# Performance work log

Hardware: AMD Instinct MI355X
Metric: run time of the kernel (lower is better)

## Reference

```python
import jax, jax.numpy as jnp
import numpy as np
from jax import lax


def _conv_layer(x, K, k, stride, pad):
    """Faithful reimplementation of the custom Conv2d, including its two quirks:
    1) weight/input flatten-order mismatch: K.reshape(k*k*cin, cout) pairs flat
       index m (decoded as kh,kw,cin for K) against x flattened as (cin,kh,kw),
       so the effective conv weight is K.reshape(-1,cout).reshape(cin,k,k,cout).
    2) the python loop range(0, padd-k, stride) misses the last valid position
       whenever (padd-k) is divisible by stride, leaving last row/col zero.
    """
    B, cin, s_in, _ = x.shape
    cout = K.shape[-1]
    out_size = (s_in + 2 * pad - k) // stride + 1
    padd = s_in + 2 * pad
    n_loop = -(-(padd - k) // stride)  # = len(range(0, padd-k, stride))
    xp = jnp.pad(x, ((0, 0), (0, 0), (pad, pad), (pad, pad))) if pad > 0 else x
    # effective weight honoring the flatten-order mismatch: (cin, kh, kw, cout)
    W = K.reshape(-1, cout).reshape(cin, k, k, cout)
    y = lax.conv_general_dilated(
        xp, W, window_strides=(stride, stride), padding='VALID',
        dimension_numbers=('NCHW', 'IHWO', 'NCHW'))
    n = min(n_loop, out_size)
    out = jnp.zeros((B, cout, out_size, out_size), x.dtype)
    out = out.at[:, :, :n, :n].set(y[:, :, :n, :n])
    return out


def setup_inputs() -> dict:
    key = jax.random.key(0)
    ks = jax.random.split(key, 9)
    NUM_CLASSES = 10
    B = 8192

    def kinit(k_, shape):
        fan_in = shape[1] * int(np.prod(shape[2:]))  # torch fan_in for 4D
        bound = float(np.sqrt(6.0 / fan_in))
        return jax.random.uniform(k_, shape, jnp.float32, -bound, bound)

    x = jax.random.normal(ks[0], (B, 3, 28, 28), jnp.float32)
    K1 = kinit(ks[1], (5, 5, 3, 8))
    K2 = kinit(ks[2], (3, 3, 8, 16))
    K3 = kinit(ks[3], (3, 3, 16, 16))
    K4 = kinit(ks[4], (3, 3, 16, 16))
    K5 = kinit(ks[5], (3, 3, 16, 16))
    K6 = kinit(ks[6], (5, 5, 16, 32))
    fc_in = 6 * 6 * 32  # 1152
    bw = float(np.sqrt(1.0 / fc_in))
    Wfc = jax.random.uniform(ks[7], (NUM_CLASSES, fc_in), jnp.float32, -bw, bw)
    bfc = jax.random.uniform(ks[8], (NUM_CLASSES,), jnp.float32, -bw, bw)
    return {"x": x, "K1": K1, "K2": K2, "K3": K3, "K4": K4, "K5": K5,
            "K6": K6, "Wfc": Wfc, "bfc": bfc}


def reference(x, K1, K2, K3, K4, K5, K6, Wfc, bfc):
    h = jax.nn.relu(_conv_layer(x, K1, 5, 2, 1))   # (B,8,13,13)
    h = jax.nn.relu(_conv_layer(h, K2, 3, 1, 1))   # (B,16,13,13), last row/col zero
    h = jax.nn.relu(_conv_layer(h, K3, 3, 1, 1))
    h = jax.nn.relu(_conv_layer(h, K4, 3, 1, 1))
    h = jax.nn.relu(_conv_layer(h, K5, 3, 1, 1))
    h = _conv_layer(h, K6, 5, 2, 1)                # (B,32,6,6), last row/col zero
    flat = h.reshape(h.shape[0], -1)               # (B,1152)
    logits = flat @ Wfc.T + bfc
    return jax.nn.softmax(logits, axis=1)
```

## Files before the change

kernel.cpp:

```cpp
#include <hip/hip_runtime.h>
#include <math.h>

#define TPB 256

typedef __attribute__((ext_vector_type(8))) short short8;
typedef __attribute__((ext_vector_type(4))) float f32x4;
typedef unsigned short u16;

__device__ __forceinline__ f32x4 MFMA(short8 a, short8 b, f32x4 c) {
    return __builtin_amdgcn_mfma_f32_16x16x32_bf16(a, b, c, 0, 0, 0);
}
__device__ __forceinline__ u16 f2bf(float f) {
    unsigned int u = __builtin_bit_cast(unsigned int, f);
    u += 0x7FFFu + ((u >> 16) & 1u);
    return (u16)(u >> 16);
}
__device__ __forceinline__ float bf2f(u16 h) {
    unsigned int u = ((unsigned int)h) << 16;
    return __builtin_bit_cast(float, u);
}

extern "C" __global__ void prep_w(const float* __restrict__ K2, const float* __restrict__ K3,
                                  const float* __restrict__ K4, const float* __restrict__ K5,
                                  const float* __restrict__ K6, short8* __restrict__ W)
{
    const int slot = blockIdx.x * blockDim.x + threadIdx.x;
    if (slot >= 5632) return;
    const int lane = slot & 63;
    const int ent  = slot >> 6;
    const int o    = lane & 15;
    const int lhi  = lane >> 4;
    float w[8];
    int hl;
    if (ent < 6) {
        const int s = ent >> 1; hl = ent & 1;
        const int t = s * 4 + lhi;
#pragma unroll
        for (int j = 0; j < 8; j++)
            w[j] = (t < 9) ? K2[(j * 9 + t) * 16 + o] : 0.f;
    } else if (ent < 36) {
        const int e  = ent - 6;
        const float* Kg = (e < 10) ? K3 : (e < 20) ? K4 : K5;
        const int el = e % 10;
        const int s  = el >> 1; hl = el & 1;
        const int chalf = (lhi & 1) * 8;
        const int t = 2 * s + (lhi >> 1);
#pragma unroll
        for (int j = 0; j < 8; j++)
            w[j] = (t < 9) ? Kg[((chalf + j) * 9 + t) * 16 + o] : 0.f;
    } else {
        const int e = ent - 36;
        const int s = e >> 2; hl = (e >> 1) & 1;
        const int nh = e & 1;
        const int chalf = (lhi & 1) * 8;
        const int t  = 2 * s + (lhi >> 1);
        const int oo = nh * 16 + o;
#pragma unroll
        for (int j = 0; j < 8; j++)
            w[j] = (t < 25) ? K6[((chalf + j) * 25 + t) * 32 + oo] : 0.f;
    }
    short8 v;
#pragma unroll
    for (int j = 0; j < 8; j++) {
        const u16 h = f2bf(w[j]);
        v[j] = hl ? (short)f2bf(w[j] - bf2f(h)) : (short)h;
    }
    W[slot] = v;
}


__device__ __forceinline__ void conv8(const u16* __restrict__ s0,
                                      u16* __restrict__ d0,
                                      const short8* __restrict__ Wt,
                                      int wave, int lane, int rot)
{
    const int o   = lane & 15;
    const int lhi = lane >> 4;
    short8 Bhi[3], Blo[3];
#pragma unroll
    for (int s = 0; s < 3; s++) {
        Bhi[s] = Wt[(s * 2 + 0) * 64 + lane];
        Blo[s] = Wt[(s * 2 + 1) * 64 + lane];
    }
    const u16* sl = s0 + 3600;
    const int r0 = lane & 15;

    auto tile = [&](int m) {
        const int p  = m * 16 + r0;
        const int ip = (p * 683) >> 13;
        const int jp = p - 12 * ip;
        f32x4 acc = {0.f, 0.f, 0.f, 0.f};
#pragma unroll
        for (int s = 0; s < 3; s++) {
            const int t  = s * 4 + lhi;
            const int tt = t > 8 ? 8 : t;
            const int kh = (tt * 11) >> 5;
            const int kw = tt - 3 * kh;
            const int px = (ip + kh) * 15 + (jp + kw);
            const short8 Ahi = *(const short8*)(s0 + px * 8);
            const short8 Alo = *(const short8*)(sl + px * 8);
            acc = MFMA(Ahi, Bhi[s], acc);
            acc = MFMA(Alo, Bhi[s], acc);
            acc = MFMA(Ahi, Blo[s], acc);
        }
        const int p0 = m * 16 + lhi * 4;
#pragma unroll
        for (int r = 0; r < 4; r++) {
            const int pp = p0 + r;
            const int ii = (pp * 683) >> 13;
            const int jj = pp - 12 * ii;
            const float v = fmaxf(acc[r], 0.f);
            const u16 h = f2bf(v);
            const int px2 = (ii + 1) * 15 + (jj + 1);
            const int da  = (o >> 3) * 1800 + px2 * 8 + (o & 7);
            d0[da]        = h;
            d0[da + 3600] = f2bf(v - bf2f(h));
        }
    };
    const int m0 = (wave + rot) & 3;
    tile(m0);
    tile(m0 + 4);
    if (m0 == 0) tile(8);
}

__device__ __forceinline__ void conv16(const u16* __restrict__ s0,
                                       u16* __restrict__ d0,
                                       const short8* __restrict__ Wt,
                                       int wave, int lane, int rot)
{
    const int o    = lane & 15;
    const int lhi  = lane >> 4;
    const int hsel = lhi & 1;
    const int tsel = lhi >> 1;
    short8 Bhi[5], Blo[5];
#pragma unroll
    for (int s = 0; s < 5; s++) {
        Bhi[s] = Wt[(s * 2 + 0) * 64 + lane];
        Blo[s] = Wt[(s * 2 + 1) * 64 + lane];
    }
    const u16* sh = s0 + hsel * 1800;
    const u16* sl = sh + 3600;
    const int r0 = lane & 15;

    auto tile = [&](int m) {
        const int p  = m * 16 + r0;
        const int ip = (p * 683) >> 13;
        const int jp = p - 12 * ip;
        f32x4 acc = {0.f, 0.f, 0.f, 0.f};
#pragma unroll
        for (int s = 0; s < 5; s++) {
            const int t  = 2 * s + tsel;
            const int tt = t > 8 ? 8 : t;
            const int kh = (tt * 11) >> 5;
            const int kw = tt - 3 * kh;
            const int px = (ip + kh) * 15 + (jp + kw);
            const short8 Ahi = *(const short8*)(sh + px * 8);
            const short8 Alo = *(const short8*)(sl + px * 8);
            acc = MFMA(Ahi, Bhi[s], acc);
            acc = MFMA(Alo, Bhi[s], acc);
            acc = MFMA(Ahi, Blo[s], acc);
        }
        const int p0 = m * 16 + lhi * 4;
#pragma unroll
        for (int r = 0; r < 4; r++) {
            const int pp = p0 + r;
            const int ii = (pp * 683) >> 13;
            const int jj = pp - 12 * ii;
            const float v = fmaxf(acc[r], 0.f);
            const u16 h = f2bf(v);
            const int px2 = (ii + 1) * 15 + (jj + 1);
            const int da  = (o >> 3) * 1800 + px2 * 8 + (o & 7);
            d0[da]        = h;
            d0[da + 3600] = f2bf(v - bf2f(h));
        }
    };
    const int m0 = (wave + rot) & 3;
    tile(m0);
    tile(m0 + 4);
    if (m0 == 0) tile(8);
}

extern "C" __global__ void __launch_bounds__(TPB)
cnn_fused(const float* __restrict__ xg, const float* __restrict__ K1,
          const float* __restrict__ Wfc, const float* __restrict__ bfc,
          const short8* __restrict__ W, float* __restrict__ out)
{
    __shared__ __align__(16) unsigned char smem[28864];
    u16*   const Ah   = (u16*)smem;
    u16*   const Bh   = (u16*)(smem + 14400);
    float* const sX   = (float*)(smem + 14400);
    float* const sF   = (float*)(smem + 14400);
    float* const sLog = (float*)(smem + 28800);
    uint4* const z4   = (uint4*)smem;
    const uint4 Z = {0u, 0u, 0u, 0u};

    const int tid  = threadIdx.x;
    const int lane = tid & 63;
    const int wave = tid >> 6;
    const int img  = blockIdx.x;

    for (int i = tid; i < 1804; i += TPB) z4[i] = Z;
    __syncthreads();

    const float4* xi4 = (const float4*)(xg + (size_t)img * 2352);
    for (int i4 = tid; i4 < 588; i4 += TPB) {
        const float4 v = xi4[i4];
        const int c = i4 / 196;
        const int rem = i4 - c * 196;
        const int r = rem / 7;
        const int q = rem - r * 7;
        float* dp = sX + c * 900 + (r + 1) * 30 + q * 4 + 1;
        dp[0] = v.x; dp[1] = v.y; dp[2] = v.z; dp[3] = v.w;
    }
    __syncthreads();

    if (tid < 208) {
        const int o  = tid & 7;
        const int jj = tid >> 3;
        const int j  = jj % 13;
        const int i0 = (jj / 13) * 7;
        float acc[7];
#pragma unroll
        for (int q = 0; q < 7; q++) acc[q] = 0.f;
#pragma unroll
        for (int c = 0; c < 3; c++) {
            const float* bp = sX + c * 900 + 2 * j;
#pragma unroll
            for (int kwp = 0; kwp < 2; kwp++) {
                float2 xr[17];
#pragma unroll
                for (int r = 0; r < 17; r++) {
                    int row = 2 * i0 + r;
                    row = row > 29 ? 29 : row;
                    xr[r] = *(const float2*)(bp + row * 30 + 2 * kwp);
                }
#pragma unroll
                for (int kh = 0; kh < 5; kh++) {
                    const float w0 = K1[(c * 25 + kh * 5 + 2 * kwp) * 8 + o];
                    const float w1 = K1[(c * 25 + kh * 5 + 2 * kwp + 1) * 8 + o];
#pragma unroll
                    for (int q = 0; q < 7; q++) {
                        acc[q] = fmaf(xr[2 * q + kh].x, w0, acc[q]);
                        acc[q] = fmaf(xr[2 * q + kh].y, w1, acc[q]);
                    }
                }
            }
            {
                float xs[17];
#pragma unroll
                for (int r = 0; r < 17; r++) {
                    int row = 2 * i0 + r;
                    row = row > 29 ? 29 : row;
                    xs[r] = bp[row * 30 + 4];
                }
#pragma unroll
                for (int kh = 0; kh < 5; kh++) {
                    const float w4 = K1[(c * 25 + kh * 5 + 4) * 8 + o];
#pragma unroll
                    for (int q = 0; q < 7; q++)
                        acc[q] = fmaf(xs[2 * q + kh], w4, acc[q]);
                }
            }
        }
#pragma unroll
        for (int q = 0; q < 7; q++) {
            const int i = i0 + q;
            if (i < 13) {
                const float v = fmaxf(acc[q], 0.f);
                const u16 h = f2bf(v);
                const int da = ((i + 1) * 15 + (j + 1)) * 8 + o;
                Ah[da]        = h;
                Ah[da + 3600] = f2bf(v - bf2f(h));
            }
        }
    }
    __syncthreads();

    for (int i = tid + 900; i < 1800; i += TPB) z4[i] = Z;
    __syncthreads();

    conv8(Ah, Bh, W, wave, lane, 0);
    __syncthreads();

    for (int i = tid; i < 900; i += TPB) z4[i] = Z;
    __syncthreads();

    conv16(Bh, Ah, W + 384, wave, lane, 1);
    __syncthreads();
    conv16(Ah, Bh, W + 1024, wave, lane, 2);
    __syncthreads();
    conv16(Bh, Ah, W + 1664, wave, lane, 3);
    __syncthreads();

    for (int i = tid + 900; i < 1188; i += TPB) z4[i] = Z;
    __syncthreads();

    {
        const short8* Wt6 = W + 2304;
        const int mt   = wave >> 1;
        const int nh   = wave & 1;
        const int lhi  = lane >> 4;
        const int hsel = lhi & 1;
        const int tsel = lhi >> 1;
        const int o    = nh * 16 + (lane & 15);
        const int pr = mt * 16 + (lane & 15);
        const int pe = pr < 25 ? pr : 0;
        const int ia = (pe * 52) >> 8;
        const int ja = pe - 5 * ia;
        const u16* sh = Ah + hsel * 1800;
        const u16* sl = sh + 3600;
        f32x4 acc = {0.f, 0.f, 0.f, 0.f};
#pragma unroll 4
        for (int s = 0; s < 13; s++) {
            const int t  = 2 * s + tsel;
            const int tt = t > 24 ? 24 : t;
            const int kh = (tt * 52) >> 8;
            const int kw = tt - 5 * kh;
            const int px = (2 * ia + kh) * 15 + (2 * ja + kw);
            const short8 Ahi = *(const short8*)(sh + px * 8);
            const short8 Alo = *(const short8*)(sl + px * 8);
            const short8 Bh2 = Wt6[((s * 2 + 0) * 2 + nh) * 64 + lane];
            const short8 Bl2 = Wt6[((s * 2 + 1) * 2 + nh) * 64 + lane];
            acc = MFMA(Ahi, Bh2, acc);
            acc = MFMA(Alo, Bh2, acc);
            acc = MFMA(Ahi, Bl2, acc);
        }
        const int p0 = mt * 16 + lhi * 4;
#pragma unroll
        for (int r = 0; r < 4; r++) {
            const int pp = p0 + r;
            if (pp < 25) {
                const int ii = (pp * 52) >> 8;
                const int jj = pp - 5 * ii;
                sF[o * 36 + ii * 6 + jj] = acc[r];
            }
        }
    }
    __syncthreads();

    if (tid < 160) {
        const int c = tid >> 4;
        const int l = tid & 15;
        const float4* fv = (const float4*)(sF + l * 72);
        const float4* wv = (const float4*)(Wfc + c * 1152 + l * 72);
        float p = 0.f;
#pragma unroll
        for (int m = 0; m < 18; m++) {
            const float4 a = fv[m];
            const float4 b = wv[m];
            p = fmaf(a.x, b.x, p);
            p = fmaf(a.y, b.y, p);
            p = fmaf(a.z, b.z, p);
            p = fmaf(a.w, b.w, p);
        }
        p += __shfl_down(p, 8, 16);
        p += __shfl_down(p, 4, 16);
        p += __shfl_down(p, 2, 16);
        p += __shfl_down(p, 1, 16);
        if (l == 0) sLog[c] = p + bfc[c];
    }
    __syncthreads();

    if (tid < 10) {
        float mx = sLog[0];
#pragma unroll
        for (int k = 1; k < 10; k++) mx = fmaxf(mx, sLog[k]);
        float s = 0.f;
#pragma unroll
        for (int k = 0; k < 10; k++) s += expf(sLog[k] - mx);
        out[(size_t)img * 10 + tid] = expf(sLog[tid] - mx) / s;
    }
}

extern "C" void kernel_launch(void* const* d_in, const int* in_sizes, int n_in,
                              void* d_out, int out_size, void* d_ws, size_t ws_size,
                              hipStream_t stream) {
    const float* x   = (const float*)d_in[0];
    const float* K1  = (const float*)d_in[1];
    const float* K2  = (const float*)d_in[2];
    const float* K3  = (const float*)d_in[3];
    const float* K4  = (const float*)d_in[4];
    const float* K5  = (const float*)d_in[5];
    const float* K6  = (const float*)d_in[6];
    const float* Wfc = (const float*)d_in[7];
    const float* bfc = (const float*)d_in[8];
    float* out = (float*)d_out;
    short8* W = (short8*)d_ws;

    prep_w<<<22, TPB, 0, stream>>>(K2, K3, K4, K5, K6, W);

    const int B = in_sizes[0] / 2352;
    cnn_fused<<<B, TPB, 0, stream>>>(x, K1, Wfc, bfc, W, out);
}
```

Measured before the change: 220.1 us.

## Move first conv layer onto bf16 split-precision MFMA with preprocessed K1 weights

Replaces the scalar FP32 FMA implementation of conv1 (5x5 stride 2, 3->8 channels) with MFMA tiles using a hi/lo bf16 split of both inputs and K1 weights. The K1 weights are packed by prep_w, and the input is stored in LDS as bf16 hi/lo planes. The LDS layout is reorganised into three buffers and some zeroing passes and barriers are removed. Shared memory grows from about 28.9KB to 40.4KB, which may reduce occupancy. Half of each MFMA's output columns and part of the K dimension are padding, so some work is wasted.

```diff
diff --git a/kernel.cpp b/kernel.cpp
--- a/kernel.cpp
+++ b/kernel.cpp
@@ -20,12 +20,13 @@
     return __builtin_bit_cast(float, u);
 }
 
-extern "C" __global__ void prep_w(const float* __restrict__ K2, const float* __restrict__ K3,
-                                  const float* __restrict__ K4, const float* __restrict__ K5,
-                                  const float* __restrict__ K6, short8* __restrict__ W)
+extern "C" __global__ void prep_w(const float* __restrict__ K1, const float* __restrict__ K2,
+                                  const float* __restrict__ K3, const float* __restrict__ K4,
+                                  const float* __restrict__ K5, const float* __restrict__ K6,
+                                  short8* __restrict__ W)
 {
     const int slot = blockIdx.x * blockDim.x + threadIdx.x;
-    if (slot >= 5632) return;
+    if (slot >= 6144) return;
     const int lane = slot & 63;
     const int ent  = slot >> 6;
     const int o    = lane & 15;
@@ -48,7 +49,7 @@
 #pragma unroll
         for (int j = 0; j < 8; j++)
             w[j] = (t < 9) ? Kg[((chalf + j) * 9 + t) * 16 + o] : 0.f;
-    } else {
+    } else if (ent < 88) {
         const int e = ent - 36;
         const int s = e >> 2; hl = (e >> 1) & 1;
         const int nh = e & 1;
@@ -58,6 +59,16 @@
 #pragma unroll
         for (int j = 0; j < 8; j++)
             w[j] = (t < 25) ? K6[((chalf + j) * 25 + t) * 32 + oo] : 0.f;
+    } else {
+        const int e = ent - 88;
+        const int s = e >> 1; hl = e & 1;
+        const int g  = s * 4 + lhi;
+        const int gc = g > 14 ? 14 : g;
+        const int c  = (gc * 52) >> 8;
+        const int kh = gc - 5 * c;
+#pragma unroll
+        for (int j = 0; j < 8; j++)
+            w[j] = (g < 15 && o < 8 && j < 5) ? K1[(c * 25 + kh * 5 + j) * 8 + o] : 0.f;
     }
     short8 v;
 #pragma unroll
@@ -181,16 +192,16 @@
 }
 
 extern "C" __global__ void __launch_bounds__(TPB)
-cnn_fused(const float* __restrict__ xg, const float* __restrict__ K1,
+cnn_fused(const float* __restrict__ xg,
           const float* __restrict__ Wfc, const float* __restrict__ bfc,
           const short8* __restrict__ W, float* __restrict__ out)
 {
-    __shared__ __align__(16) unsigned char smem[28864];
-    u16*   const Ah   = (u16*)smem;
-    u16*   const Bh   = (u16*)(smem + 14400);
-    float* const sX   = (float*)(smem + 14400);
-    float* const sF   = (float*)(smem + 14400);
-    float* const sLog = (float*)(smem + 28800);
+    __shared__ __align__(16) unsigned char smem[40384];
+    u16*   const Sh   = (u16*)smem;
+    u16*   const Ah   = (u16*)(smem + 11520);
+    u16*   const Bhp  = (u16*)(smem + 25920);
+    float* const sF   = (float*)smem;
+    float* const sLog = (float*)(smem + 40320);
     uint4* const z4   = (uint4*)smem;
     const uint4 Z = {0u, 0u, 0u, 0u};
 
@@ -199,7 +210,7 @@
     const int wave = tid >> 6;
     const int img  = blockIdx.x;
 
-    for (int i = tid; i < 1804; i += TPB) z4[i] = Z;
+    for (int i = tid; i < 2524; i += TPB) z4[i] = Z;
     __syncthreads();
 
     const float4* xi4 = (const float4*)(xg + (size_t)img * 2352);
@@ -209,90 +220,73 @@
         const int rem = i4 - c * 196;
         const int r = rem / 7;
         const int q = rem - r * 7;
-        float* dp = sX + c * 900 + (r + 1) * 30 + q * 4 + 1;
-        dp[0] = v.x; dp[1] = v.y; dp[2] = v.z; dp[3] = v.w;
-    }
-    __syncthreads();
-
-    if (tid < 208) {
-        const int o  = tid & 7;
-        const int jj = tid >> 3;
-        const int j  = jj % 13;
-        const int i0 = (jj / 13) * 7;
-        float acc[7];
-#pragma unroll
-        for (int q = 0; q < 7; q++) acc[q] = 0.f;
-#pragma unroll
-        for (int c = 0; c < 3; c++) {
-            const float* bp = sX + c * 900 + 2 * j;
-#pragma unroll
-            for (int kwp = 0; kwp < 2; kwp++) {
-                float2 xr[17];
-#pragma unroll
-                for (int r = 0; r < 17; r++) {
-                    int row = 2 * i0 + r;
-                    row = row > 29 ? 29 : row;
-                    xr[r] = *(const float2*)(bp + row * 30 + 2 * kwp);
-                }
-#pragma unroll
-                for (int kh = 0; kh < 5; kh++) {
-                    const float w0 = K1[(c * 25 + kh * 5 + 2 * kwp) * 8 + o];
-                    const float w1 = K1[(c * 25 + kh * 5 + 2 * kwp + 1) * 8 + o];
-#pragma unroll
-                    for (int q = 0; q < 7; q++) {
-                        acc[q] = fmaf(xr[2 * q + kh].x, w0, acc[q]);
-                        acc[q] = fmaf(xr[2 * q + kh].y, w1, acc[q]);
-                    }
+        const int ad = c * 960 + (r + 1) * 32 + q * 4 + 1;
+        const float vv[4] = {v.x, v.y, v.z, v.w};
+#pragma unroll
+        for (int e = 0; e < 4; e++) {
+            const u16 h = f2bf(vv[e]);
+            Sh[ad + e]        = h;
+            Sh[ad + e + 2880] = f2bf(vv[e] - bf2f(h));
+        }
+    }
+    __syncthreads();
+
+    {
+        const short8* Wt1 = W + 5632;
+        const int o   = lane & 15;
+        const int lhi = lane >> 4;
+        short8 B1h[4], B1l[4];
+#pragma unroll
+        for (int s = 0; s < 4; s++) {
+            B1h[s] = Wt1[(s * 2 + 0) * 64 + lane];
+            B1l[s] = Wt1[(s * 2 + 1) * 64 + lane];
+        }
+        const u16* slo = Sh + 2880;
+        for (int m = wave; m < 11; m += 4) {
+            const int p  = m * 16 + o;
+            const int pc = p > 168 ? 168 : p;
+            const int i = (pc * 316) >> 12;
+            const int j = pc - 13 * i;
+            f32x4 acc = {0.f, 0.f, 0.f, 0.f};
+#pragma unroll
+            for (int s = 0; s < 4; s++) {
+                const int g  = s * 4 + lhi;
+                const int gc = g > 14 ? 14 : g;
+                const int c  = (gc * 52) >> 8;
+                const int kh = gc - 5 * c;
+                const int ad = c * 960 + (2 * i + kh) * 32 + 2 * j;
+                const short8 Ahi = *(const short8*)(Sh + ad);
+                const short8 Alo = *(const short8*)(slo + ad);
+                acc = MFMA(Ahi, B1h[s], acc);
+                acc = MFMA(Alo, B1h[s], acc);
+                acc = MFMA(Ahi, B1l[s], acc);
+            }
+#pragma unroll
+            for (int r = 0; r < 4; r++) {
+                const int pp = m * 16 + lhi * 4 + r;
+                if (pp < 169 && o < 8) {
+                    const int ii = (pp * 316) >> 12;
+                    const int jj = pp - 13 * ii;
+                    const float v = fmaxf(acc[r], 0.f);
+                    const u16 h = f2bf(v);
+                    const int da = ((ii + 1) * 15 + (jj + 1)) * 8 + o;
+                    Bhp[da]        = h;
+                    Bhp[da + 3600] = f2bf(v - bf2f(h));
                 }
             }
-            {
-                float xs[17];
-#pragma unroll
-                for (int r = 0; r < 17; r++) {
-                    int row = 2 * i0 + r;
-                    row = row > 29 ? 29 : row;
-                    xs[r] = bp[row * 30 + 4];
-                }
-#pragma unroll
-                for (int kh = 0; kh < 5; kh++) {
-                    const float w4 = K1[(c * 25 + kh * 5 + 4) * 8 + o];
-#pragma unroll
-                    for (int q = 0; q < 7; q++)
-                        acc[q] = fmaf(xs[2 * q + kh], w4, acc[q]);
-                }
-            }
-        }
-#pragma unroll
-        for (int q = 0; q < 7; q++) {
-            const int i = i0 + q;
-            if (i < 13) {
-                const float v = fmaxf(acc[q], 0.f);
-                const u16 h = f2bf(v);
-                const int da = ((i + 1) * 15 + (j + 1)) * 8 + o;
-                Ah[da]        = h;
-                Ah[da + 3600] = f2bf(v - bf2f(h));
-            }
-        }
-    }
-    __syncthreads();
-
-    for (int i = tid + 900; i < 1800; i += TPB) z4[i] = Z;
-    __syncthreads();
-
-    conv8(Ah, Bh, W, wave, lane, 0);
-    __syncthreads();
-
-    for (int i = tid; i < 900; i += TPB) z4[i] = Z;
-    __syncthreads();
-
-    conv16(Bh, Ah, W + 384, wave, lane, 1);
-    __syncthreads();
-    conv16(Ah, Bh, W + 1024, wave, lane, 2);
-    __syncthreads();
-    conv16(Bh, Ah, W + 1664, wave, lane, 3);
-    __syncthreads();
-
-    for (int i = tid + 900; i < 1188; i += TPB) z4[i] = Z;
+        }
+    }
+    __syncthreads();
+
+    for (int i = tid; i < 288; i += TPB) z4[i] = Z;
+
+    conv8(Bhp, Ah, W, wave, lane, 0);
+    __syncthreads();
+    conv16(Ah, Bhp, W + 384, wave, lane, 1);
+    __syncthreads();
+    conv16(Bhp, Ah, W + 1024, wave, lane, 2);
+    __syncthreads();
+    conv16(Ah, Bhp, W + 1664, wave, lane, 3);
     __syncthreads();
 
     {
@@ -307,7 +301,7 @@
         const int pe = pr < 25 ? pr : 0;
         const int ia = (pe * 52) >> 8;
         const int ja = pe - 5 * ia;
-        const u16* sh = Ah + hsel * 1800;
+        const u16* sh = Bhp + hsel * 1800;
         const u16* sl = sh + 3600;
         f32x4 acc = {0.f, 0.f, 0.f, 0.f};
 #pragma unroll 4
@@ -387,8 +381,8 @@
     float* out = (float*)d_out;
     short8* W = (short8*)d_ws;
 
-    prep_w<<<22, TPB, 0, stream>>>(K2, K3, K4, K5, K6, W);
+    prep_w<<<24, TPB, 0, stream>>>(K1, K2, K3, K4, K5, K6, W);
 
     const int B = in_sizes[0] / 2352;
-    cnn_fused<<<B, TPB, 0, stream>>>(x, K1, Wfc, bfc, W, out);
-}
+    cnn_fused<<<B, TPB, 0, stream>>>(x, Wfc, bfc, W, out);
+}
```

Result: faster. 213.6 us (-3.0%).
